# Performance work log

Measured on AMD Instinct MI355X. Metric: run time of the kernel, lower is better.

The kernel has to match this reference:

```python
import jax, jax.numpy as jnp
import numpy as np

B, N, K = 4, 8192, 32
HID, INP = 64, 64
IN_CH = HID + INP  # 128; SetConv fc1 sees IN_CH + 3 (relative pos)


def setup_inputs() -> dict:
    key = jax.random.key(0)
    ks = jax.random.split(key, 10)
    return {
        "h": jax.random.normal(ks[0], (B, N, HID), jnp.float32),
        "x": jax.random.normal(ks[1], (B, N, INP), jnp.float32),
        "c": jax.random.normal(ks[2], (B, N, 3), jnp.float32),
        "W1": jax.random.normal(ks[3], (3, IN_CH + 3, HID), jnp.float32) * 0.05,
        "b1": jnp.zeros((3, HID), jnp.float32),
        "W2": jax.random.normal(ks[4], (3, HID, HID), jnp.float32) * 0.05,
        "b2": jnp.zeros((3, HID), jnp.float32),
        "W3": jax.random.normal(ks[5], (3, HID, HID), jnp.float32) * 0.05,
        "b3": jnp.zeros((3, HID), jnp.float32),
        "neigh_idx": jax.random.randint(ks[6], (B, N, K), 0, N, jnp.int32),
        "edge_feats": jax.random.normal(ks[7], (B, N, K, 3), jnp.float32),
    }


def reference(h, x, c, W1, b1, W2, b2, W3, b3, neigh_idx, edge_feats):
    # c (point coordinates) is unused by the GRU body, matching the torch source.
    slope = 0.1

    def setconv(i, feat):
        # gather K neighbor features per point: [B, N, K, C]
        g = jax.vmap(lambda fb, ib: fb[ib])(feat, neigh_idx)
        e = jnp.concatenate([g, edge_feats], axis=-1)  # [B, N, K, C+3]
        y = jax.nn.leaky_relu(jnp.einsum('bnkc,cd->bnkd', e, W1[i]) + b1[i], slope)
        y = y.max(axis=2)  # pool over neighbors -> [B, N, HID]
        y = jax.nn.leaky_relu(y @ W2[i] + b2[i], slope)
        return y @ W3[i] + b3[i]

    hx = jnp.concatenate([h, x], axis=2)
    z = jax.nn.sigmoid(setconv(0, hx))
    r = jax.nn.sigmoid(setconv(1, hx))
    q = jnp.tanh(setconv(2, jnp.concatenate([r * h, x], axis=2)))
    return (1.0 - z) * h + z * q
```

## Files before the change

kernel.cpp:

```cpp
#include <hip/hip_runtime.h>
#include <math.h>

typedef unsigned short u16;
typedef unsigned int u32;

#define KNBR 32

__device__ __forceinline__ float bf2f(u16 u) { return __uint_as_float((u32)u << 16); }
__device__ __forceinline__ float bflo(u32 u) { return __uint_as_float(u << 16); }
__device__ __forceinline__ float bfhi(u32 u) { return __uint_as_float(u & 0xffff0000u); }
__device__ __forceinline__ u16 f2bf(float f) {
    u32 u = __float_as_uint(f);
    return (u16)((u + 0x7fffu + ((u >> 16) & 1u)) >> 16);
}
__device__ __forceinline__ u32 pk2(float a, float b) {
    return (u32)f2bf(a) | ((u32)f2bf(b) << 16);
}
__device__ __forceinline__ float leaky(float v) { return v >= 0.f ? v : 0.1f * v; }
__device__ __forceinline__ float sigm(float v) { return 1.f / (1.f + expf(-v)); }


__global__ __launch_bounds__(512) void k_gemm_p01(
    const float* __restrict__ h, const float* __restrict__ x,
    const float* __restrict__ W1f, const float* __restrict__ b1f,
    u32* __restrict__ P01, int p0)
{
    __shared__ u32 a_lds[128 * 65];
    __shared__ float w_lds[2][64 * 64];
    int t = threadIdx.x;
    int plb = blockIdx.x * 128;
    int pgb = p0 + plb;
    for (int i = 0; i < 16; ++i) {
        int id = t + i * 512;
        int p = id >> 6, cw = id & 63;
        const float* src = (cw < 32) ? (h + (size_t)(pgb + p) * 64 + cw * 2)
                                     : (x + (size_t)(pgb + p) * 64 + (cw - 32) * 2);
        float2 v = *(const float2*)src;
        a_lds[p * 65 + cw] = pk2(v.x, v.y);
    }
    int lane = t & 63;
    int cg = __builtin_amdgcn_readfirstlane(t >> 6);
    int di = lane & 15, pi = lane >> 4;
    int pt0 = cg * 16 + pi * 4;
    int dch = di * 4;
    float acc0[4][4], acc1[4][4];
    float4 bv0 = *(const float4*)&b1f[dch];
    float4 bv1 = *(const float4*)&b1f[64 + dch];
    #pragma unroll
    for (int pp = 0; pp < 4; ++pp) {
        acc0[pp][0] = bv0.x; acc0[pp][1] = bv0.y; acc0[pp][2] = bv0.z; acc0[pp][3] = bv0.w;
        acc1[pp][0] = bv1.x; acc1[pp][1] = bv1.y; acc1[pp][2] = bv1.z; acc1[pp][3] = bv1.w;
    }
    for (int half = 0; half < 2; ++half) {
        __syncthreads();
        for (int i = 0; i < 4; ++i) {
            int id = t + i * 512;
            int g = id >> 10, r = (id >> 4) & 63, d4 = id & 15;
            *(float4*)&w_lds[g][r * 64 + d4 * 4] =
                *(const float4*)(W1f + g * 8384 + (half * 64 + r) * 64 + d4 * 4);
        }
        __syncthreads();
        #pragma unroll 2
        for (int cw = 0; cw < 32; ++cw) {
            u32 aw[4];
            #pragma unroll
            for (int pp = 0; pp < 4; ++pp) aw[pp] = a_lds[(pt0 + pp) * 65 + half * 32 + cw];
            float4 wa0 = *(float4*)&w_lds[0][(2 * cw) * 64 + dch];
            float4 wa1 = *(float4*)&w_lds[0][(2 * cw + 1) * 64 + dch];
            float4 wb0 = *(float4*)&w_lds[1][(2 * cw) * 64 + dch];
            float4 wb1 = *(float4*)&w_lds[1][(2 * cw + 1) * 64 + dch];
            #pragma unroll
            for (int pp = 0; pp < 4; ++pp) {
                float a0 = bflo(aw[pp]), a1 = bfhi(aw[pp]);
                acc0[pp][0] = fmaf(a0, wa0.x, acc0[pp][0]);
                acc0[pp][1] = fmaf(a0, wa0.y, acc0[pp][1]);
                acc0[pp][2] = fmaf(a0, wa0.z, acc0[pp][2]);
                acc0[pp][3] = fmaf(a0, wa0.w, acc0[pp][3]);
                acc0[pp][0] = fmaf(a1, wa1.x, acc0[pp][0]);
                acc0[pp][1] = fmaf(a1, wa1.y, acc0[pp][1]);
                acc0[pp][2] = fmaf(a1, wa1.z, acc0[pp][2]);
                acc0[pp][3] = fmaf(a1, wa1.w, acc0[pp][3]);
                acc1[pp][0] = fmaf(a0, wb0.x, acc1[pp][0]);
                acc1[pp][1] = fmaf(a0, wb0.y, acc1[pp][1]);
                acc1[pp][2] = fmaf(a0, wb0.z, acc1[pp][2]);
                acc1[pp][3] = fmaf(a0, wb0.w, acc1[pp][3]);
                acc1[pp][0] = fmaf(a1, wb1.x, acc1[pp][0]);
                acc1[pp][1] = fmaf(a1, wb1.y, acc1[pp][1]);
                acc1[pp][2] = fmaf(a1, wb1.z, acc1[pp][2]);
                acc1[pp][3] = fmaf(a1, wb1.w, acc1[pp][3]);
            }
        }
    }
    #pragma unroll
    for (int pp = 0; pp < 4; ++pp) {
        u32 o[4];
        #pragma unroll
        for (int j = 0; j < 4; ++j) o[j] = pk2(acc0[pp][j], acc1[pp][j]);
        *(uint4*)(P01 + (size_t)(plb + pt0 + pp) * 64 + dch) = *(uint4*)o;
    }
}

__global__ __launch_bounds__(512) void k_fuse01(
    const u32* __restrict__ P01, const float* __restrict__ W1f,
    const int* __restrict__ nidx, const float* __restrict__ ef,
    const float* __restrict__ h, const float* __restrict__ x,
    const float* __restrict__ W2f, const float* __restrict__ b2f,
    const float* __restrict__ W3f, const float* __restrict__ b3f,
    const float* __restrict__ b1f,
    u16* __restrict__ Z, u16* __restrict__ P2, int p0)
{
    __shared__ u32 a_lds[64 * 65];
    __shared__ float w_lds[2][64 * 64];
    int t = threadIdx.x;
    int plb = blockIdx.x * 64;
    int lane = t & 63;
    int cg = __builtin_amdgcn_readfirstlane(t >> 6);

    for (int i = 0; i < 4; ++i) {
        int id = t + i * 512;
        int g = id >> 10, r = (id >> 4) & 63, d4 = id & 15;
        *(float4*)&w_lds[g][r * 64 + d4 * 4] =
            *(const float4*)(W2f + g * 4096 + r * 64 + d4 * 4);
    }
    {
        u16* y16 = (u16*)a_lds;
        float w00 = W1f[8192 + lane], w01 = W1f[8256 + lane], w02 = W1f[8320 + lane];
        float w10 = W1f[16576 + lane], w11 = W1f[16640 + lane], w12 = W1f[16704 + lane];
        for (int pp = 0; pp < 8; ++pp) {
            int lp = cg * 8 + pp;
            int pg = p0 + plb + lp;
            int rbase = ((pg >> 13) << 13) - p0;
            const int* ni = nidx + (size_t)pg * KNBR;
            const float* ep = ef + (size_t)pg * KNBR * 3;
            float m0 = -1e30f, m1 = -1e30f;
            #pragma unroll 16
            for (int k = 0; k < KNBR; ++k) {
                int lr = rbase + ni[k];
                u32 g = P01[(size_t)lr * 64 + lane];
                float e0 = ep[3 * k], e1 = ep[3 * k + 1], e2 = ep[3 * k + 2];
                m0 = fmaxf(m0, bflo(g) + e0 * w00 + e1 * w01 + e2 * w02);
                m1 = fmaxf(m1, bfhi(g) + e0 * w10 + e1 * w11 + e2 * w12);
            }
            y16[lp * 130 + lane]      = f2bf(leaky(m0));
            y16[lp * 130 + 64 + lane] = f2bf(leaky(m1));
        }
    }
    __syncthreads();
    int g = cg >> 2, q = cg & 3;
    int di = lane & 15, pi = lane >> 4;
    int pt0 = q * 16 + pi * 4;
    int dch = di * 4;
    float acc[4][4];
    {
        float4 bv = *(const float4*)&b2f[g * 64 + dch];
        #pragma unroll
        for (int pp = 0; pp < 4; ++pp) {
            acc[pp][0] = bv.x; acc[pp][1] = bv.y; acc[pp][2] = bv.z; acc[pp][3] = bv.w;
        }
    }
    #pragma unroll 2
    for (int cw = 0; cw < 32; ++cw) {
        u32 aw[4];
        #pragma unroll
        for (int pp = 0; pp < 4; ++pp) aw[pp] = a_lds[(pt0 + pp) * 65 + g * 32 + cw];
        float4 w0 = *(float4*)&w_lds[g][(2 * cw) * 64 + dch];
        float4 w1 = *(float4*)&w_lds[g][(2 * cw + 1) * 64 + dch];
        #pragma unroll
        for (int pp = 0; pp < 4; ++pp) {
            float a0 = bflo(aw[pp]), a1 = bfhi(aw[pp]);
            acc[pp][0] = fmaf(a0, w0.x, acc[pp][0]);
            acc[pp][1] = fmaf(a0, w0.y, acc[pp][1]);
            acc[pp][2] = fmaf(a0, w0.z, acc[pp][2]);
            acc[pp][3] = fmaf(a0, w0.w, acc[pp][3]);
            acc[pp][0] = fmaf(a1, w1.x, acc[pp][0]);
            acc[pp][1] = fmaf(a1, w1.y, acc[pp][1]);
            acc[pp][2] = fmaf(a1, w1.z, acc[pp][2]);
            acc[pp][3] = fmaf(a1, w1.w, acc[pp][3]);
        }
    }
    __syncthreads();
    #pragma unroll
    for (int pp = 0; pp < 4; ++pp) {
        int base = (pt0 + pp) * 65 + g * 32 + di * 2;
        a_lds[base]     = pk2(leaky(acc[pp][0]), leaky(acc[pp][1]));
        a_lds[base + 1] = pk2(leaky(acc[pp][2]), leaky(acc[pp][3]));
    }
    for (int i = 0; i < 4; ++i) {
        int id = t + i * 512;
        int gg = id >> 10, r = (id >> 4) & 63, d4 = id & 15;
        *(float4*)&w_lds[gg][r * 64 + d4 * 4] =
            *(const float4*)(W3f + gg * 4096 + r * 64 + d4 * 4);
    }
    __syncthreads();
    {
        float4 bv = *(const float4*)&b3f[g * 64 + dch];
        #pragma unroll
        for (int pp = 0; pp < 4; ++pp) {
            acc[pp][0] = bv.x; acc[pp][1] = bv.y; acc[pp][2] = bv.z; acc[pp][3] = bv.w;
        }
    }
    #pragma unroll 2
    for (int cw = 0; cw < 32; ++cw) {
        u32 aw[4];
        #pragma unroll
        for (int pp = 0; pp < 4; ++pp) aw[pp] = a_lds[(pt0 + pp) * 65 + g * 32 + cw];
        float4 w0 = *(float4*)&w_lds[g][(2 * cw) * 64 + dch];
        float4 w1 = *(float4*)&w_lds[g][(2 * cw + 1) * 64 + dch];
        #pragma unroll
        for (int pp = 0; pp < 4; ++pp) {
            float a0 = bflo(aw[pp]), a1 = bfhi(aw[pp]);
            acc[pp][0] = fmaf(a0, w0.x, acc[pp][0]);
            acc[pp][1] = fmaf(a0, w0.y, acc[pp][1]);
            acc[pp][2] = fmaf(a0, w0.z, acc[pp][2]);
            acc[pp][3] = fmaf(a0, w0.w, acc[pp][3]);
            acc[pp][0] = fmaf(a1, w1.x, acc[pp][0]);
            acc[pp][1] = fmaf(a1, w1.y, acc[pp][1]);
            acc[pp][2] = fmaf(a1, w1.z, acc[pp][2]);
            acc[pp][3] = fmaf(a1, w1.w, acc[pp][3]);
        }
    }
    __syncthreads();
    if (g == 0) {
        #pragma unroll
        for (int pp = 0; pp < 4; ++pp) {
            int pl = plb + pt0 + pp;
            uint2 o;
            o.x = pk2(sigm(acc[pp][0]), sigm(acc[pp][1]));
            o.y = pk2(sigm(acc[pp][2]), sigm(acc[pp][3]));
            *(uint2*)(Z + (size_t)pl * 64 + dch) = o;
        }
    } else {
        #pragma unroll
        for (int pp = 0; pp < 4; ++pp) {
            int pg = p0 + plb + pt0 + pp;
            float4 hv = *(const float4*)&h[(size_t)pg * 64 + dch];
            int base = (pt0 + pp) * 65 + di * 2;
            a_lds[base]     = pk2(sigm(acc[pp][0]) * hv.x, sigm(acc[pp][1]) * hv.y);
            a_lds[base + 1] = pk2(sigm(acc[pp][2]) * hv.z, sigm(acc[pp][3]) * hv.w);
        }
    }
    for (int i = 0; i < 4; ++i) {
        int id = t + i * 512;
        int p = id >> 5, cw = id & 31;
        float2 v = *(const float2*)(x + (size_t)(p0 + plb + p) * 64 + cw * 2);
        a_lds[p * 65 + 32 + cw] = pk2(v.x, v.y);
    }
    float* wflat = (float*)w_lds;
    for (int i = 0; i < 4; ++i) {
        int id = t + i * 512;
        int r = id >> 4, d4 = id & 15;
        *(float4*)&wflat[r * 64 + d4 * 4] =
            *(const float4*)(W1f + 2 * 8384 + r * 64 + d4 * 4);
    }
    __syncthreads();
    int pt0b = cg * 8 + pi * 2;
    float pacc[2][4];
    {
        float4 bv = *(const float4*)&b1f[128 + dch];
        #pragma unroll
        for (int pp = 0; pp < 2; ++pp) {
            pacc[pp][0] = bv.x; pacc[pp][1] = bv.y; pacc[pp][2] = bv.z; pacc[pp][3] = bv.w;
        }
    }
    #pragma unroll 2
    for (int cw = 0; cw < 64; ++cw) {
        u32 aw0 = a_lds[(pt0b + 0) * 65 + cw];
        u32 aw1 = a_lds[(pt0b + 1) * 65 + cw];
        float4 w0 = *(float4*)&wflat[(2 * cw) * 64 + dch];
        float4 w1 = *(float4*)&wflat[(2 * cw + 1) * 64 + dch];
        float a00 = bflo(aw0), a01 = bfhi(aw0);
        float a10 = bflo(aw1), a11 = bfhi(aw1);
        pacc[0][0] = fmaf(a00, w0.x, pacc[0][0]); pacc[0][1] = fmaf(a00, w0.y, pacc[0][1]);
        pacc[0][2] = fmaf(a00, w0.z, pacc[0][2]); pacc[0][3] = fmaf(a00, w0.w, pacc[0][3]);
        pacc[0][0] = fmaf(a01, w1.x, pacc[0][0]); pacc[0][1] = fmaf(a01, w1.y, pacc[0][1]);
        pacc[0][2] = fmaf(a01, w1.z, pacc[0][2]); pacc[0][3] = fmaf(a01, w1.w, pacc[0][3]);
        pacc[1][0] = fmaf(a10, w0.x, pacc[1][0]); pacc[1][1] = fmaf(a10, w0.y, pacc[1][1]);
        pacc[1][2] = fmaf(a10, w0.z, pacc[1][2]); pacc[1][3] = fmaf(a10, w0.w, pacc[1][3]);
        pacc[1][0] = fmaf(a11, w1.x, pacc[1][0]); pacc[1][1] = fmaf(a11, w1.y, pacc[1][1]);
        pacc[1][2] = fmaf(a11, w1.z, pacc[1][2]); pacc[1][3] = fmaf(a11, w1.w, pacc[1][3]);
    }
    #pragma unroll
    for (int pp = 0; pp < 2; ++pp) {
        int pl = plb + pt0b + pp;
        uint2 o;
        o.x = pk2(pacc[pp][0], pacc[pp][1]);
        o.y = pk2(pacc[pp][2], pacc[pp][3]);
        *(uint2*)(P2 + (size_t)pl * 64 + dch) = o;
    }
}

__global__ __launch_bounds__(512) void k_fuse2(
    const u16* __restrict__ P2, const float* __restrict__ W1f,
    const int* __restrict__ nidx, const float* __restrict__ ef,
    const float* __restrict__ W2f, const float* __restrict__ b2f,
    const float* __restrict__ W3f, const float* __restrict__ b3f,
    const float* __restrict__ h, const u16* __restrict__ Z,
    float* __restrict__ out, int p0)
{
    __shared__ u32 a_lds[64 * 33];
    __shared__ float w_lds[64 * 64];
    int t = threadIdx.x;
    int plb = blockIdx.x * 64;
    int lane = t & 63;
    int cg = __builtin_amdgcn_readfirstlane(t >> 6);
    for (int i = 0; i < 2; ++i) {
        int id = t + i * 512;
        int r = (id >> 4) & 63, d4 = id & 15;
        *(float4*)&w_lds[r * 64 + d4 * 4] =
            *(const float4*)(W2f + 2 * 4096 + r * 64 + d4 * 4);
    }
    {
        const float* W = W1f + 2 * 8384;
        float w0 = W[8192 + lane], w1 = W[8256 + lane], w2 = W[8320 + lane];
        u16* y16 = (u16*)a_lds;
        for (int pp = 0; pp < 8; ++pp) {
            int lp = cg * 8 + pp;
            int pg = p0 + plb + lp;
            int rbase = ((pg >> 13) << 13) - p0;
            const int* ni = nidx + (size_t)pg * KNBR;
            const float* ep = ef + (size_t)pg * KNBR * 3;
            float m = -1e30f;
            #pragma unroll 16
            for (int k = 0; k < KNBR; ++k) {
                int lr = rbase + ni[k];
                float e0 = ep[3 * k], e1 = ep[3 * k + 1], e2 = ep[3 * k + 2];
                float v = bf2f(P2[(size_t)lr * 64 + lane]) + e0 * w0 + e1 * w1 + e2 * w2;
                m = fmaxf(m, v);
            }
            y16[lp * 66 + lane] = f2bf(leaky(m));
        }
    }
    __syncthreads();
    int di = lane & 15, pi = lane >> 4;
    int pt0 = cg * 8 + pi * 2;
    int dch = di * 4;
    float acc[2][4];
    {
        float4 bv = *(const float4*)&b2f[128 + dch];
        #pragma unroll
        for (int pp = 0; pp < 2; ++pp) {
            acc[pp][0] = bv.x; acc[pp][1] = bv.y; acc[pp][2] = bv.z; acc[pp][3] = bv.w;
        }
    }
    #pragma unroll 2
    for (int cw = 0; cw < 32; ++cw) {
        u32 aw0 = a_lds[(pt0 + 0) * 33 + cw];
        u32 aw1 = a_lds[(pt0 + 1) * 33 + cw];
        float4 w0 = *(float4*)&w_lds[(2 * cw) * 64 + dch];
        float4 w1 = *(float4*)&w_lds[(2 * cw + 1) * 64 + dch];
        float a00 = bflo(aw0), a01 = bfhi(aw0);
        float a10 = bflo(aw1), a11 = bfhi(aw1);
        acc[0][0] = fmaf(a00, w0.x, acc[0][0]); acc[0][1] = fmaf(a00, w0.y, acc[0][1]);
        acc[0][2] = fmaf(a00, w0.z, acc[0][2]); acc[0][3] = fmaf(a00, w0.w, acc[0][3]);
        acc[0][0] = fmaf(a01, w1.x, acc[0][0]); acc[0][1] = fmaf(a01, w1.y, acc[0][1]);
        acc[0][2] = fmaf(a01, w1.z, acc[0][2]); acc[0][3] = fmaf(a01, w1.w, acc[0][3]);
        acc[1][0] = fmaf(a10, w0.x, acc[1][0]); acc[1][1] = fmaf(a10, w0.y, acc[1][1]);
        acc[1][2] = fmaf(a10, w0.z, acc[1][2]); acc[1][3] = fmaf(a10, w0.w, acc[1][3]);
        acc[1][0] = fmaf(a11, w1.x, acc[1][0]); acc[1][1] = fmaf(a11, w1.y, acc[1][1]);
        acc[1][2] = fmaf(a11, w1.z, acc[1][2]); acc[1][3] = fmaf(a11, w1.w, acc[1][3]);
    }
    __syncthreads();
    #pragma unroll
    for (int pp = 0; pp < 2; ++pp) {
        int base = (pt0 + pp) * 33 + di * 2;
        a_lds[base]     = pk2(leaky(acc[pp][0]), leaky(acc[pp][1]));
        a_lds[base + 1] = pk2(leaky(acc[pp][2]), leaky(acc[pp][3]));
    }
    for (int i = 0; i < 2; ++i) {
        int id = t + i * 512;
        int r = (id >> 4) & 63, d4 = id & 15;
        *(float4*)&w_lds[r * 64 + d4 * 4] =
            *(const float4*)(W3f + 2 * 4096 + r * 64 + d4 * 4);
    }
    __syncthreads();
    {
        float4 bv = *(const float4*)&b3f[128 + dch];
        #pragma unroll
        for (int pp = 0; pp < 2; ++pp) {
            acc[pp][0] = bv.x; acc[pp][1] = bv.y; acc[pp][2] = bv.z; acc[pp][3] = bv.w;
        }
    }
    #pragma unroll 2
    for (int cw = 0; cw < 32; ++cw) {
        u32 aw0 = a_lds[(pt0 + 0) * 33 + cw];
        u32 aw1 = a_lds[(pt0 + 1) * 33 + cw];
        float4 w0 = *(float4*)&w_lds[(2 * cw) * 64 + dch];
        float4 w1 = *(float4*)&w_lds[(2 * cw + 1) * 64 + dch];
        float a00 = bflo(aw0), a01 = bfhi(aw0);
        float a10 = bflo(aw1), a11 = bfhi(aw1);
        acc[0][0] = fmaf(a00, w0.x, acc[0][0]); acc[0][1] = fmaf(a00, w0.y, acc[0][1]);
        acc[0][2] = fmaf(a00, w0.z, acc[0][2]); acc[0][3] = fmaf(a00, w0.w, acc[0][3]);
        acc[0][0] = fmaf(a01, w1.x, acc[0][0]); acc[0][1] = fmaf(a01, w1.y, acc[0][1]);
        acc[0][2] = fmaf(a01, w1.z, acc[0][2]); acc[0][3] = fmaf(a01, w1.w, acc[0][3]);
        acc[1][0] = fmaf(a10, w0.x, acc[1][0]); acc[1][1] = fmaf(a10, w0.y, acc[1][1]);
        acc[1][2] = fmaf(a10, w0.z, acc[1][2]); acc[1][3] = fmaf(a10, w0.w, acc[1][3]);
        acc[1][0] = fmaf(a11, w1.x, acc[1][0]); acc[1][1] = fmaf(a11, w1.y, acc[1][1]);
        acc[1][2] = fmaf(a11, w1.z, acc[1][2]); acc[1][3] = fmaf(a11, w1.w, acc[1][3]);
    }
    #pragma unroll
    for (int pp = 0; pp < 2; ++pp) {
        int pl = plb + pt0 + pp;
        int pg = p0 + pl;
        float4 hv = *(const float4*)&h[(size_t)pg * 64 + dch];
        uint2 zw = *(const uint2*)(Z + (size_t)pl * 64 + dch);
        float z0 = bflo(zw.x), z1 = bfhi(zw.x), z2 = bflo(zw.y), z3 = bfhi(zw.y);
        float4 o;
        o.x = (1.f - z0) * hv.x + z0 * tanhf(acc[pp][0]);
        o.y = (1.f - z1) * hv.y + z1 * tanhf(acc[pp][1]);
        o.z = (1.f - z2) * hv.z + z2 * tanhf(acc[pp][2]);
        o.w = (1.f - z3) * hv.w + z3 * tanhf(acc[pp][3]);
        *(float4*)&out[(size_t)pg * 64 + dch] = o;
    }
}

extern "C" void kernel_launch(void* const* d_in, const int* in_sizes, int n_in,
                              void* d_out, int out_size, void* d_ws, size_t ws_size,
                              hipStream_t stream)
{
    const float* h  = (const float*)d_in[0];
    const float* x  = (const float*)d_in[1];
    const float* W1 = (const float*)d_in[3];
    const float* b1 = (const float*)d_in[4];
    const float* W2 = (const float*)d_in[5];
    const float* b2 = (const float*)d_in[6];
    const float* W3 = (const float*)d_in[7];
    const float* b3 = (const float*)d_in[8];
    const int* nidx = (const int*)d_in[9];
    const float* ef = (const float*)d_in[10];
    float* out = (float*)d_out;

    char* wsb = (char*)d_ws;
    size_t PN = (ws_size >= 32768ull * 512ull) ? 32768 : 8192;
    int passes = (int)(32768 / PN);

    u32* P01 = (u32*)wsb;
    u16* Z   = (u16*)(wsb + PN * 256);
    u16* P2  = (u16*)(wsb + PN * 384);

    for (int s = 0; s < passes; ++s) {
        int p0 = (int)(s * PN);
        k_gemm_p01<<<dim3((unsigned)(PN / 128)), 512, 0, stream>>>(h, x, W1, b1, P01, p0);
        k_fuse01  <<<dim3((unsigned)(PN / 64)),  512, 0, stream>>>(P01, W1, nidx, ef, h, x,
                                                                   W2, b2, W3, b3, b1, Z, P2, p0);
        k_fuse2   <<<dim3((unsigned)(PN / 64)),  512, 0, stream>>>(P2, W1, nidx, ef,
                                                                   W2, b2, W3, b3, h, Z, out, p0);
    }
}
```

Before: 198.8 us.

## Swizzle block-to-point mapping per XCD and shrink gemm tile to 64 points

Adds an XCD-aware block index swizzle so blocks on each XCD (blockIdx mod 8) work on points from one batch, keeping each batch's neighbour gathers local to one L2. The first GEMM kernel's tile drops from 128 to 64 points per block so all three kernels share the same grid and mapping. The smaller tile doubles the block count and halves register accumulators per thread, but reloads the weights into LDS twice as often.

New measurement: 199.9 us. About the same (+0.6%).

```diff
diff --git a/kernel.cpp b/kernel.cpp
--- a/kernel.cpp
+++ b/kernel.cpp
@@ -19,18 +19,25 @@
 __device__ __forceinline__ float leaky(float v) { return v >= 0.f ? v : 0.1f * v; }
 __device__ __forceinline__ float sigm(float v) { return 1.f / (1.f + expf(-v)); }
 
+__device__ __forceinline__ int swz_plb(int b, int full) {
+    if (!full) return b << 6;
+    int xcd = b & 7;
+    int within = ((b >> 3) << 1) | (xcd & 1);
+    return ((xcd >> 1) << 13) + (within << 6);
+}
+
 
 __global__ __launch_bounds__(512) void k_gemm_p01(
     const float* __restrict__ h, const float* __restrict__ x,
     const float* __restrict__ W1f, const float* __restrict__ b1f,
-    u32* __restrict__ P01, int p0)
+    u32* __restrict__ P01, int p0, int full)
 {
-    __shared__ u32 a_lds[128 * 65];
+    __shared__ u32 a_lds[64 * 65];
     __shared__ float w_lds[2][64 * 64];
     int t = threadIdx.x;
-    int plb = blockIdx.x * 128;
+    int plb = swz_plb(blockIdx.x, full);
     int pgb = p0 + plb;
-    for (int i = 0; i < 16; ++i) {
+    for (int i = 0; i < 8; ++i) {
         int id = t + i * 512;
         int p = id >> 6, cw = id & 63;
         const float* src = (cw < 32) ? (h + (size_t)(pgb + p) * 64 + cw * 2)
@@ -41,13 +48,13 @@
     int lane = t & 63;
     int cg = __builtin_amdgcn_readfirstlane(t >> 6);
     int di = lane & 15, pi = lane >> 4;
-    int pt0 = cg * 16 + pi * 4;
+    int pt0 = cg * 8 + pi * 2;
     int dch = di * 4;
-    float acc0[4][4], acc1[4][4];
+    float acc0[2][4], acc1[2][4];
     float4 bv0 = *(const float4*)&b1f[dch];
     float4 bv1 = *(const float4*)&b1f[64 + dch];
     #pragma unroll
-    for (int pp = 0; pp < 4; ++pp) {
+    for (int pp = 0; pp < 2; ++pp) {
         acc0[pp][0] = bv0.x; acc0[pp][1] = bv0.y; acc0[pp][2] = bv0.z; acc0[pp][3] = bv0.w;
         acc1[pp][0] = bv1.x; acc1[pp][1] = bv1.y; acc1[pp][2] = bv1.z; acc1[pp][3] = bv1.w;
     }
@@ -60,39 +67,36 @@
                 *(const float4*)(W1f + g * 8384 + (half * 64 + r) * 64 + d4 * 4);
         }
         __syncthreads();
-        #pragma unroll 2
+        #pragma unroll 4
         for (int cw = 0; cw < 32; ++cw) {
-            u32 aw[4];
-            #pragma unroll
-            for (int pp = 0; pp < 4; ++pp) aw[pp] = a_lds[(pt0 + pp) * 65 + half * 32 + cw];
+            u32 aw0 = a_lds[(pt0 + 0) * 65 + half * 32 + cw];
+            u32 aw1 = a_lds[(pt0 + 1) * 65 + half * 32 + cw];
             float4 wa0 = *(float4*)&w_lds[0][(2 * cw) * 64 + dch];
             float4 wa1 = *(float4*)&w_lds[0][(2 * cw + 1) * 64 + dch];
             float4 wb0 = *(float4*)&w_lds[1][(2 * cw) * 64 + dch];
             float4 wb1 = *(float4*)&w_lds[1][(2 * cw + 1) * 64 + dch];
-            #pragma unroll
-            for (int pp = 0; pp < 4; ++pp) {
-                float a0 = bflo(aw[pp]), a1 = bfhi(aw[pp]);
-                acc0[pp][0] = fmaf(a0, wa0.x, acc0[pp][0]);
-                acc0[pp][1] = fmaf(a0, wa0.y, acc0[pp][1]);
-                acc0[pp][2] = fmaf(a0, wa0.z, acc0[pp][2]);
-                acc0[pp][3] = fmaf(a0, wa0.w, acc0[pp][3]);
-                acc0[pp][0] = fmaf(a1, wa1.x, acc0[pp][0]);
-                acc0[pp][1] = fmaf(a1, wa1.y, acc0[pp][1]);
-                acc0[pp][2] = fmaf(a1, wa1.z, acc0[pp][2]);
-                acc0[pp][3] = fmaf(a1, wa1.w, acc0[pp][3]);
-                acc1[pp][0] = fmaf(a0, wb0.x, acc1[pp][0]);
-                acc1[pp][1] = fmaf(a0, wb0.y, acc1[pp][1]);
-                acc1[pp][2] = fmaf(a0, wb0.z, acc1[pp][2]);
-                acc1[pp][3] = fmaf(a0, wb0.w, acc1[pp][3]);
-                acc1[pp][0] = fmaf(a1, wb1.x, acc1[pp][0]);
-                acc1[pp][1] = fmaf(a1, wb1.y, acc1[pp][1]);
-                acc1[pp][2] = fmaf(a1, wb1.z, acc1[pp][2]);
-                acc1[pp][3] = fmaf(a1, wb1.w, acc1[pp][3]);
-            }
-        }
-    }
-    #pragma unroll
-    for (int pp = 0; pp < 4; ++pp) {
+            float a00 = bflo(aw0), a01 = bfhi(aw0);
+            float a10 = bflo(aw1), a11 = bfhi(aw1);
+            acc0[0][0] = fmaf(a00, wa0.x, acc0[0][0]); acc0[0][1] = fmaf(a00, wa0.y, acc0[0][1]);
+            acc0[0][2] = fmaf(a00, wa0.z, acc0[0][2]); acc0[0][3] = fmaf(a00, wa0.w, acc0[0][3]);
+            acc0[0][0] = fmaf(a01, wa1.x, acc0[0][0]); acc0[0][1] = fmaf(a01, wa1.y, acc0[0][1]);
+            acc0[0][2] = fmaf(a01, wa1.z, acc0[0][2]); acc0[0][3] = fmaf(a01, wa1.w, acc0[0][3]);
+            acc0[1][0] = fmaf(a10, wa0.x, acc0[1][0]); acc0[1][1] = fmaf(a10, wa0.y, acc0[1][1]);
+            acc0[1][2] = fmaf(a10, wa0.z, acc0[1][2]); acc0[1][3] = fmaf(a10, wa0.w, acc0[1][3]);
+            acc0[1][0] = fmaf(a11, wa1.x, acc0[1][0]); acc0[1][1] = fmaf(a11, wa1.y, acc0[1][1]);
+            acc0[1][2] = fmaf(a11, wa1.z, acc0[1][2]); acc0[1][3] = fmaf(a11, wa1.w, acc0[1][3]);
+            acc1[0][0] = fmaf(a00, wb0.x, acc1[0][0]); acc1[0][1] = fmaf(a00, wb0.y, acc1[0][1]);
+            acc1[0][2] = fmaf(a00, wb0.z, acc1[0][2]); acc1[0][3] = fmaf(a00, wb0.w, acc1[0][3]);
+            acc1[0][0] = fmaf(a01, wb1.x, acc1[0][0]); acc1[0][1] = fmaf(a01, wb1.y, acc1[0][1]);
+            acc1[0][2] = fmaf(a01, wb1.z, acc1[0][2]); acc1[0][3] = fmaf(a01, wb1.w, acc1[0][3]);
+            acc1[1][0] = fmaf(a10, wb0.x, acc1[1][0]); acc1[1][1] = fmaf(a10, wb0.y, acc1[1][1]);
+            acc1[1][2] = fmaf(a10, wb0.z, acc1[1][2]); acc1[1][3] = fmaf(a10, wb0.w, acc1[1][3]);
+            acc1[1][0] = fmaf(a11, wb1.x, acc1[1][0]); acc1[1][1] = fmaf(a11, wb1.y, acc1[1][1]);
+            acc1[1][2] = fmaf(a11, wb1.z, acc1[1][2]); acc1[1][3] = fmaf(a11, wb1.w, acc1[1][3]);
+        }
+    }
+    #pragma unroll
+    for (int pp = 0; pp < 2; ++pp) {
         u32 o[4];
         #pragma unroll
         for (int j = 0; j < 4; ++j) o[j] = pk2(acc0[pp][j], acc1[pp][j]);
@@ -107,12 +111,12 @@
     const float* __restrict__ W2f, const float* __restrict__ b2f,
     const float* __restrict__ W3f, const float* __restrict__ b3f,
     const float* __restrict__ b1f,
-    u16* __restrict__ Z, u16* __restrict__ P2, int p0)
+    u16* __restrict__ Z, u16* __restrict__ P2, int p0, int full)
 {
     __shared__ u32 a_lds[64 * 65];
     __shared__ float w_lds[2][64 * 64];
     int t = threadIdx.x;
-    int plb = blockIdx.x * 64;
+    int plb = swz_plb(blockIdx.x, full);
     int lane = t & 63;
     int cg = __builtin_amdgcn_readfirstlane(t >> 6);
 
@@ -295,12 +299,12 @@
     const float* __restrict__ W2f, const float* __restrict__ b2f,
     const float* __restrict__ W3f, const float* __restrict__ b3f,
     const float* __restrict__ h, const u16* __restrict__ Z,
-    float* __restrict__ out, int p0)
+    float* __restrict__ out, int p0, int full)
 {
     __shared__ u32 a_lds[64 * 33];
     __shared__ float w_lds[64 * 64];
     int t = threadIdx.x;
-    int plb = blockIdx.x * 64;
+    int plb = swz_plb(blockIdx.x, full);
     int lane = t & 63;
     int cg = __builtin_amdgcn_readfirstlane(t >> 6);
     for (int i = 0; i < 2; ++i) {
@@ -432,6 +436,7 @@
     char* wsb = (char*)d_ws;
     size_t PN = (ws_size >= 32768ull * 512ull) ? 32768 : 8192;
     int passes = (int)(32768 / PN);
+    int full = (PN == 32768) ? 1 : 0;
 
     u32* P01 = (u32*)wsb;
     u16* Z   = (u16*)(wsb + PN * 256);
@@ -439,10 +444,11 @@
 
     for (int s = 0; s < passes; ++s) {
         int p0 = (int)(s * PN);
-        k_gemm_p01<<<dim3((unsigned)(PN / 128)), 512, 0, stream>>>(h, x, W1, b1, P01, p0);
-        k_fuse01  <<<dim3((unsigned)(PN / 64)),  512, 0, stream>>>(P01, W1, nidx, ef, h, x,
-                                                                   W2, b2, W3, b3, b1, Z, P2, p0);
-        k_fuse2   <<<dim3((unsigned)(PN / 64)),  512, 0, stream>>>(P2, W1, nidx, ef,
-                                                                   W2, b2, W3, b3, h, Z, out, p0);
-    }
-}
+        dim3 g((unsigned)(PN / 64));
+        k_gemm_p01<<<g, 512, 0, stream>>>(h, x, W1, b1, P01, p0, full);
+        k_fuse01  <<<g, 512, 0, stream>>>(P01, W1, nidx, ef, h, x,
+                                          W2, b2, W3, b3, b1, Z, P2, p0, full);
+        k_fuse2   <<<g, 512, 0, stream>>>(P2, W1, nidx, ef,
+                                          W2, b2, W3, b3, h, Z, out, p0, full);
+    }
+}
```
